# Optimization experiments

Hardware: AMD Instinct MI355X
Metric: run time of the kernel (lower is better)

Reference implementation:

```python
import jax, jax.numpy as jnp
import numpy as np

B, S, HID = 2, 2048, 2048
H, HKV, HD = 16, 8, 128
INPUT_CHUNK, RET_CHUNK = 256, 64
NUM_CHUNKS = S // INPUT_CHUNK - 1          # 7 retrieval chunks
INPUT_START = NUM_CHUNKS * RET_CHUNK       # 448
KV_LEN = S + INPUT_START                   # 2496
SCALE = HD ** -0.5


def _document_id():
    d = np.zeros(KV_LEN, np.int32)
    d[INPUT_START:] = -1
    for i in range(NUM_CHUNKS):            # retrieval chunks get ids 1..NUM_CHUNKS
        d[RET_CHUNK * i: RET_CHUNK * (i + 1)] = i + 1
    for i in range(1, NUM_CHUNKS + 1):     # input chunk i (i>=1) gets id i
        d[INPUT_START + INPUT_CHUNK * i: INPUT_START + INPUT_CHUNK * (i + 1)] = i
    return d


def _causal_retrieval_mask():
    d = _document_id()
    q = np.arange(S)[:, None]
    kv = np.arange(KV_LEN)[None, :]
    causal = (q + INPUT_START >= kv) & (kv > INPUT_START)
    docm = (d[q + INPUT_START] == d[kv]) & (kv < INPUT_START)
    return jnp.asarray(causal | docm)      # [S, KV_LEN] bool


_MASK = _causal_retrieval_mask()


def rotate_half(x):
    x1, x2 = jnp.split(x, 2, axis=-1)
    return jnp.concatenate([-x2, x1], axis=-1)


def setup_inputs() -> dict:
    key = jax.random.key(0)
    ks = jax.random.split(key, 8)
    hidden_states = jax.random.normal(ks[0], (B, S, HID), jnp.float32)
    # standard llama RoPE tables
    pos = jnp.arange(S, dtype=jnp.float32)
    inv = 1.0 / (10000.0 ** (jnp.arange(0, HD, 2, dtype=jnp.float32) / HD))
    f = pos[:, None] * inv[None, :]
    emb = jnp.concatenate([f, f], axis=-1)
    cos = jnp.broadcast_to(jnp.cos(emb), (B, S, HD)).astype(jnp.float32)
    sin = jnp.broadcast_to(jnp.sin(emb), (B, S, HD)).astype(jnp.float32)
    retrieval_key_states = jax.random.normal(ks[1], (B * NUM_CHUNKS, HKV, RET_CHUNK, HD), jnp.float32)
    retrieval_value_states = jax.random.normal(ks[2], (B * NUM_CHUNKS, HKV, RET_CHUNK, HD), jnp.float32)
    s = 0.02
    Wq = jax.random.normal(ks[3], (HID, H * HD), jnp.float32) * s
    Wk = jax.random.normal(ks[4], (HID, HKV * HD), jnp.float32) * s
    Wv = jax.random.normal(ks[5], (HID, HKV * HD), jnp.float32) * s
    Wo = jax.random.normal(ks[6], (H * HD, HID), jnp.float32) * s
    return {"hidden_states": hidden_states, "cos": cos, "sin": sin,
            "retrieval_key_states": retrieval_key_states,
            "retrieval_value_states": retrieval_value_states,
            "Wq": Wq, "Wk": Wk, "Wv": Wv, "Wo": Wo}


def reference(hidden_states, cos, sin, retrieval_key_states, retrieval_value_states, Wq, Wk, Wv, Wo):
    b = hidden_states.shape[0]
    # QKV projections (bias=False), -> [b, h, s, d]
    q = (hidden_states @ Wq).reshape(b, S, H, HD).transpose(0, 2, 1, 3)
    k = (hidden_states @ Wk).reshape(b, S, HKV, HD).transpose(0, 2, 1, 3)
    v = (hidden_states @ Wv).reshape(b, S, HKV, HD).transpose(0, 2, 1, 3)
    # RoPE (cos/sin unsqueezed over heads)
    c = cos[:, None]
    sn = sin[:, None]
    q = q * c + rotate_half(q) * sn
    k = k * c + rotate_half(k) * sn
    # retrieval KV: (b*nc, hkv, rc, d) -> (b, hkv, nc*rc, d)
    rk = retrieval_key_states.reshape(b, NUM_CHUNKS, HKV, RET_CHUNK, HD).transpose(0, 2, 1, 3, 4).reshape(b, HKV, NUM_CHUNKS * RET_CHUNK, HD)
    rv = retrieval_value_states.reshape(b, NUM_CHUNKS, HKV, RET_CHUNK, HD).transpose(0, 2, 1, 3, 4).reshape(b, HKV, NUM_CHUNKS * RET_CHUNK, HD)
    k_all = jnp.concatenate([rk, k], axis=2)     # [b, hkv, KV_LEN, d]
    v_all = jnp.concatenate([rv, v], axis=2)
    # GQA: repeat kv heads
    g = H // HKV
    k_all = jnp.repeat(k_all, g, axis=1)
    v_all = jnp.repeat(v_all, g, axis=1)
    scores = jnp.einsum('bhqd,bhkd->bhqk', q, k_all) * SCALE
    neg = jnp.finfo(scores.dtype).min
    scores = jnp.where(_MASK[None, None], scores, neg)
    probs = jax.nn.softmax(scores, axis=-1)
    # fully-masked rows (q_idx=0) -> 0 output, matching flex_attention semantics
    probs = jnp.where(_MASK[None, None], probs, 0.0)
    attn = jnp.einsum('bhqk,bhkd->bhqd', probs, v_all)   # [b, H, S, HD]
    # NOTE: source reshapes (b, H, S, HD) directly to (b, S, H*HD) with NO transpose
    attn = attn.reshape(b, S, H * HD)
    return attn @ Wo
```

## Files before the change

### kernel.cpp

```cpp
#include <hip/hip_runtime.h>

#define B_ 2
#define S_ 2048
#define HID_ 2048
#define H_ 16
#define HKV_ 8
#define HD_ 128
#define NCH_ 7
#define RET_ 64
#define IST_ 448
#define KVL_ 2496
#define SCALE_ 0.08838834764831845f
#define SC2_ (0.08838834764831845f * 1.44269504088896340f)
#define MCAP_ 16.0f

typedef __attribute__((ext_vector_type(8))) short short8;
typedef __attribute__((ext_vector_type(4))) float f32x4;

static __device__ __forceinline__ unsigned short f2bf(float f) {
    unsigned u = __float_as_uint(f);
    unsigned r = (u + 0x7fffu + ((u >> 16) & 1u)) >> 16;
    return (unsigned short)r;
}
static __device__ __forceinline__ float bf2f(unsigned short x) {
    return __uint_as_float(((unsigned)x) << 16);
}

#define GLL16(gp, lp) __builtin_amdgcn_global_load_lds( \
    (__attribute__((address_space(1))) void*)(void*)(gp), \
    (__attribute__((address_space(3))) void*)(void*)(lp), 16, 0, 0)

__global__ __launch_bounds__(256) void cvt_f32_bf16(const float* __restrict__ x,
                                                    unsigned short* __restrict__ y, int n4) {
    int i = blockIdx.x * 256 + threadIdx.x;
    if (i >= n4) return;
    float4 v = ((const float4*)x)[i];
    ushort4 o;
    o.x = f2bf(v.x); o.y = f2bf(v.y); o.z = f2bf(v.z); o.w = f2bf(v.w);
    ((ushort4*)y)[i] = o;
}

__global__ void transpose_all(const float* __restrict__ Wq, const float* __restrict__ Wk,
                              const float* __restrict__ Wv, const float* __restrict__ Wo,
                              unsigned short* __restrict__ wqkvT, unsigned short* __restrict__ woT) {
    __shared__ float t[32][33];
    const int z = blockIdx.z;
    const float* W;
    unsigned short* WT;
    int N;
    if (z == 0)      { W = Wq; WT = wqkvT;                        N = 2048; }
    else if (z == 1) { W = Wk; WT = wqkvT + (size_t)2048 * 2048;  N = 1024; }
    else if (z == 2) { W = Wv; WT = wqkvT + (size_t)3072 * 2048;  N = 1024; }
    else             { W = Wo; WT = woT;                          N = 2048; }
    const int k0 = blockIdx.x << 5, n0 = blockIdx.y << 5;
    if (n0 >= N) return;
    const int tx = threadIdx.x, ty = threadIdx.y;
#pragma unroll
    for (int i = 0; i < 4; i++)
        t[ty + i * 8][tx] = W[(size_t)(k0 + ty + i * 8) * N + n0 + tx];
    __syncthreads();
#pragma unroll
    for (int i = 0; i < 4; i++)
        WT[(size_t)(n0 + ty + i * 8) * 2048 + k0 + tx] = f2bf(t[tx][ty + i * 8]);
}

template <int BN, typename OT>
__global__ __launch_bounds__(512, 2) void gemm256(const unsigned short* __restrict__ A,
                                                  const unsigned short* __restrict__ BT,
                                                  OT* __restrict__ C,
                                                  int M, int N, int K) {
    constexpr int NJ = BN / 64;
    __shared__ short As[2][16384];
    __shared__ short Bs[2][BN * 64];
    const int tid = threadIdx.x;
    const int wid = tid >> 6, lane = tid & 63;
    const int lq = lane & 15, lk = lane >> 4;
    const int wm = wid >> 2, wn = wid & 3;
    const int bm = blockIdx.x, bn = blockIdx.y;

    const int rowin = tid >> 3;
    const int koff = (((tid & 7) ^ (rowin & 7)) << 3);
    const size_t abase = (size_t)(bm * 256 + rowin) * K;
    const size_t bbase = (size_t)(bn * BN + rowin) * K;
    const int ldst = wid * 512;

    f32x4 acc[8][NJ] = {};

    auto stage = [&](int buf, int k0) {
#pragma unroll
        for (int r = 0; r < 4; r++)
            GLL16(A + abase + (size_t)(r * 64) * K + k0 + koff, &As[buf][r * 4096 + ldst]);
#pragma unroll
        for (int r = 0; r < NJ; r++)
            GLL16(BT + bbase + (size_t)(r * 64) * K + k0 + koff, &Bs[buf][r * 4096 + ldst]);
    };

    const int nk = K >> 6;
    stage(0, 0);
    __syncthreads();
    for (int t = 0; t < nk; t++) {
        const int cur = t & 1;
        if (t + 1 < nk) stage(cur ^ 1, (t + 1) << 6);
        short8 bf[2][NJ];
#pragma unroll
        for (int j = 0; j < NJ; j++)
#pragma unroll
            for (int kk = 0; kk < 2; kk++) {
                const int row = wn * (BN / 4) + j * 16 + lq;
                bf[kk][j] = *(const short8*)&Bs[cur][row * 64 +
                                                     (((kk * 4 + lk) ^ (lq & 7)) << 3)];
            }
#pragma unroll
        for (int p = 0; p < 4; p++) {
            short8 af0[2], af1[2];
#pragma unroll
            for (int kk = 0; kk < 2; kk++) {
                const int r0 = wm * 128 + (2 * p) * 16 + lq;
                const int r1 = wm * 128 + (2 * p + 1) * 16 + lq;
                af0[kk] = *(const short8*)&As[cur][r0 * 64 +
                                                   (((kk * 4 + lk) ^ (lq & 7)) << 3)];
                af1[kk] = *(const short8*)&As[cur][r1 * 64 +
                                                   (((kk * 4 + lk) ^ (lq & 7)) << 3)];
            }
            __builtin_amdgcn_s_setprio(1);
#pragma unroll
            for (int j = 0; j < NJ; j++)
#pragma unroll
                for (int kk = 0; kk < 2; kk++) {
                    acc[2 * p][j] =
                        __builtin_amdgcn_mfma_f32_16x16x32_bf16(bf[kk][j], af0[kk], acc[2 * p][j], 0, 0, 0);
                    acc[2 * p + 1][j] =
                        __builtin_amdgcn_mfma_f32_16x16x32_bf16(bf[kk][j], af1[kk], acc[2 * p + 1][j], 0, 0, 0);
                }
            __builtin_amdgcn_s_setprio(0);
        }
        __syncthreads();
    }
#pragma unroll
    for (int i = 0; i < 8; i++) {
        const size_t row = (size_t)(bm * 256 + wm * 128 + i * 16 + lq);
#pragma unroll
        for (int j = 0; j < NJ; j++) {
            const size_t col = (size_t)(bn * BN + wn * (BN / 4) + j * 16 + lk * 4);
            if constexpr (sizeof(OT) == 2) {
                ushort4 u;
                u.x = f2bf(acc[i][j][0]);
                u.y = f2bf(acc[i][j][1]);
                u.z = f2bf(acc[i][j][2]);
                u.w = f2bf(acc[i][j][3]);
                *(ushort4*)&C[row * N + col] = u;
            } else {
                *(f32x4*)&C[row * N + col] = acc[i][j];
            }
        }
    }
}

__global__ __launch_bounds__(256) void prep_k_kernel(const unsigned short* __restrict__ qkvraw,
                                                     const float* __restrict__ cosb,
                                                     const float* __restrict__ sinb,
                                                     const float* __restrict__ rk,
                                                     unsigned short* __restrict__ kall) {
    const int bid = blockIdx.x;
    if (bid < 8192) {
        size_t idx = (size_t)bid * 256 + threadIdx.x;
        int d = idx & 63;
        int hk = (idx >> 6) & 7;
        size_t bs = idx >> 9;
        size_t base = bs * 4096 + 2048 + hk * 128 + d;
        int b = (int)(bs >> 11), s = (int)(bs & 2047);
        float x1 = bf2f(qkvraw[base]), x2 = bf2f(qkvraw[base + 64]);
        float c1 = cosb[(size_t)s * 128 + d], sn1 = sinb[(size_t)s * 128 + d];
        float c2 = cosb[(size_t)s * 128 + d + 64], sn2 = sinb[(size_t)s * 128 + d + 64];
        size_t o = ((size_t)(b * HKV_ + hk) * KVL_ + IST_ + s) * HD_ + d;
        kall[o] = f2bf(x1 * c1 - x2 * sn1);
        kall[o + 64] = f2bf(x2 * c2 + x1 * sn2);
    } else {
        size_t idx = (size_t)(bid - 8192) * 256 + threadIdx.x;
        int d = idx & 127;
        int r = (idx >> 7) & 63;
        int hk = (idx >> 13) & 7;
        int bc = (int)(idx >> 16);
        int b = bc / NCH_, ch = bc % NCH_;
        kall[((size_t)(b * HKV_ + hk) * KVL_ + ch * RET_ + r) * HD_ + d] = f2bf(rk[idx]);
    }
}

__global__ void prep_v_kernel(const unsigned short* __restrict__ qkvraw,
                              const float* __restrict__ rv,
                              unsigned short* __restrict__ vt) {
    const int bid = blockIdx.x;
    const int tx = threadIdx.x, ty = threadIdx.y;
    if (bid < 4096) {
        __shared__ unsigned short t[32][33];
        const int d0 = (bid & 3) << 5, s0 = ((bid >> 2) & 63) << 5;
        const int bh = bid >> 8;
        const int b = bh >> 3, hk = bh & 7;
#pragma unroll
        for (int i = 0; i < 4; i++)
            t[ty + i * 8][tx] =
                qkvraw[(size_t)(b * S_ + s0 + ty + i * 8) * 4096 + 3072 + hk * 128 + d0 + tx];
        __syncthreads();
#pragma unroll
        for (int i = 0; i < 4; i++)
            vt[((size_t)(b * HKV_ + hk) * HD_ + d0 + ty + i * 8) * KVL_ + IST_ + s0 + tx] =
                t[tx][ty + i * 8];
    } else {
        __shared__ float tf[32][33];
        const int bid2 = bid - 4096;
        const int d0 = (bid2 & 3) << 5;
        const int r0 = ((bid2 >> 2) & 1) << 5;
        const int z = bid2 >> 3;
        const int bc = z >> 3, hk = z & 7;
        const int b = bc / NCH_, ch = bc % NCH_;
#pragma unroll
        for (int i = 0; i < 4; i++)
            tf[ty + i * 8][tx] =
                rv[((size_t)(bc * HKV_ + hk) * RET_ + r0 + ty + i * 8) * HD_ + d0 + tx];
        __syncthreads();
#pragma unroll
        for (int i = 0; i < 4; i++)
            vt[((size_t)(b * HKV_ + hk) * HD_ + d0 + ty + i * 8) * KVL_ + ch * RET_ + r0 + tx] =
                f2bf(tf[tx][ty + i * 8]);
    }
}

__global__ __launch_bounds__(1024) void attn_kernel(const unsigned short* __restrict__ qkvraw,
                                                    const unsigned short* __restrict__ kall,
                                                    const unsigned short* __restrict__ vt,
                                                    const float* __restrict__ cosb,
                                                    const float* __restrict__ sinb,
                                                    unsigned short* __restrict__ attnb) {
    __shared__ short Ks[2][8192];
    __shared__ short Vs[2][8192];
    __shared__ short Ps[16][1024];
    const int tid = threadIdx.x;
    const int wid = tid >> 6, lane = tid & 63;
    const int lq = lane & 15, lk = lane >> 4;
    const int pairi = blockIdx.x;
    const int h = blockIdx.y, b = blockIdx.z, hk = h >> 1;
    const unsigned short* kbase = kall + (size_t)(b * HKV_ + hk) * KVL_ * HD_;
    const unsigned short* vbase = vt + (size_t)(b * HKV_ + hk) * HD_ * KVL_;

    const int so = tid * 16;
    const int krow = so >> 8;
    const int koffe = (((tid & 15) ^ (krow & 7)) << 3);
    const int vrow = so >> 7;
    const unsigned short* vrp = vbase + (size_t)vrow * KVL_ + (((tid & 7) ^ (vrow & 7)) << 3);
    short* psw = &Ps[wid][0];

    const int qlo = pairi * 128, qhi = (15 - pairi) * 128;
    const int wgrp = wid >> 3;
    const int qb0 = wgrp ? qhi : qlo;
    const int qbw = qb0 + (wid & 7) * 16;
    const int mydoc = qb0 >> 8;
    const int doc_lo = qlo >> 8;
    const int doc_hi = qhi >> 8;
    const int nr = (doc_lo >= 1 ? 2 : 1);
    const int nt = nr + (qhi + 128) / 64;

    const unsigned short* qrp = qkvraw + ((size_t)(b * S_) + qbw + lq) * 4096 + h * 128;
    short8 qr[4];
#pragma unroll
    for (int d = 0; d < 4; d++) qr[d] = *(const short8*)(qrp + d * 32 + lk * 8);
    const float* cosp = cosb + (size_t)(qbw + lq) * 128 + lk * 8;
    const float* sinp = sinb + (size_t)(qbw + lq) * 128 + lk * 8;
    short8 qf[4];
#pragma unroll
    for (int d = 0; d < 4; d++) {
        float4 c0 = *(const float4*)(cosp + d * 32);
        float4 c1 = *(const float4*)(cosp + d * 32 + 4);
        float4 s0 = *(const float4*)(sinp + d * 32);
        float4 s1 = *(const float4*)(sinp + d * 32 + 4);
        const float cc[8] = {c0.x, c0.y, c0.z, c0.w, c1.x, c1.y, c1.z, c1.w};
        const float ss[8] = {s0.x, s0.y, s0.z, s0.w, s1.x, s1.y, s1.z, s1.w};
        const int od = d ^ 2;
        const float sg = (d < 2) ? -1.f : 1.f;
#pragma unroll
        for (int e = 0; e < 8; e++) {
            float x = bf2f((unsigned short)qr[d][e]);
            float y = bf2f((unsigned short)qr[od][e]);
            qf[d][e] = (short)f2bf(fmaf(sg * y, ss[e], x * cc[e]));
        }
    }

    f32x4 o[8] = {};
    float lsump = 0.f;

    auto kvof = [&](int t) -> int {
        if (t < nr) return (nr == 2 && t == 0) ? RET_ * (doc_lo - 1) : RET_ * (doc_hi - 1);
        return IST_ + (t - nr) * 64;
    };
    auto stage = [&](int buf, int kv0) {
        GLL16(kbase + (size_t)(kv0 + krow) * HD_ + koffe, &Ks[buf][wid * 512]);
        GLL16(vrp + kv0, &Vs[buf][wid * 512]);
    };

    stage(0, kvof(0));
    asm volatile("s_waitcnt vmcnt(0)" ::: "memory");
    __syncthreads();
    int cur = 0;
    for (int t = 0; t < nt; t++) {
        if (t + 1 < nt) stage(cur ^ 1, kvof(t + 1));
        const int kv0 = kvof(t);
        const bool isret = (kv0 < IST_);
        const bool active = isret ? (mydoc >= 1 && kv0 == RET_ * (mydoc - 1))
                                  : (kv0 <= qbw + 15 + IST_);
        if (active) {
            const bool needMask = !isret && !((kv0 != IST_) && (kv0 + 63 <= qbw + IST_));
            const char* kb = (const char*)&Ks[cur][0];
            const char* vb = (const char*)&Vs[cur][0];
            f32x4 sa[4] = {};
            __builtin_amdgcn_s_setprio(1);
#pragma unroll
            for (int d = 0; d < 4; d++) {
#pragma unroll
                for (int j = 0; j < 4; j++) {
                    short8 kf = *(const short8*)(kb + ((j * 16 + lq) * 256 +
                                                       (((d * 4 + lk) ^ (lq & 7)) << 4)));
                    sa[j] = __builtin_amdgcn_mfma_f32_16x16x32_bf16(kf, qf[d], sa[j], 0, 0, 0);
                }
            }
            __builtin_amdgcn_s_setprio(0);

            if (needMask) {
                const int qg = qbw + lq;
#pragma unroll
                for (int j = 0; j < 4; j++)
#pragma unroll
                    for (int r = 0; r < 4; r++) {
                        int kg = kv0 + j * 16 + lk * 4 + r;
                        if (!(kg > IST_ && kg <= qg + IST_)) sa[j][r] = -3e38f;
                    }
            }
#pragma unroll
            for (int j = 0; j < 4; j++) {
                float p0 = __builtin_amdgcn_exp2f(fmaf(sa[j][0], SC2_, -MCAP_));
                float p1 = __builtin_amdgcn_exp2f(fmaf(sa[j][1], SC2_, -MCAP_));
                float p2 = __builtin_amdgcn_exp2f(fmaf(sa[j][2], SC2_, -MCAP_));
                float p3 = __builtin_amdgcn_exp2f(fmaf(sa[j][3], SC2_, -MCAP_));
                lsump += (p0 + p1) + (p2 + p3);
                uint2 w;
                w.x = ((unsigned)f2bf(p1) << 16) | f2bf(p0);
                w.y = ((unsigned)f2bf(p3) << 16) | f2bf(p2);
                *(uint2*)((char*)psw + (lq * 128 + ((j * 32 + lk * 8) ^ ((lq & 7) << 4)))) = w;
            }
            __builtin_amdgcn_s_setprio(1);
#pragma unroll
            for (int ks = 0; ks < 2; ks++) {
                short8 pa = *(const short8*)((const char*)psw +
                                             (lq * 128 + (((ks * 4 + lk) ^ (lq & 7)) << 4)));
#pragma unroll
                for (int db = 0; db < 8; db++) {
                    short8 vf = *(const short8*)(vb + ((db * 16 + lq) * 128 +
                                                       (((ks * 4 + lk) ^ (lq & 7)) << 4)));
                    o[db] = __builtin_amdgcn_mfma_f32_16x16x32_bf16(pa, vf, o[db], 0, 0, 0);
                }
            }
            __builtin_amdgcn_s_setprio(0);
        }
        if (t + 1 < nt) asm volatile("s_waitcnt vmcnt(0)" ::: "memory");
        __syncthreads();
        cur ^= 1;
    }

    float ls = lsump;
    ls += __shfl_xor(ls, 16);
    ls += __shfl_xor(ls, 32);
    float inv[4];
#pragma unroll
    for (int r = 0; r < 4; r++) {
        float v = __shfl(ls, lk * 4 + r);
        inv[r] = v > 0.f ? 1.f / v : 0.f;
    }
#pragma unroll
    for (int db = 0; db < 8; db++)
#pragma unroll
        for (int r = 0; r < 4; r++) {
            int qg = qbw + lk * 4 + r;
            size_t row = (size_t)b * 2048 + h * 128 + (qg >> 4);
            size_t col = (size_t)(qg & 15) * 128 + db * 16 + lq;
            attnb[row * 2048 + col] = f2bf(o[db][r] * inv[r]);
        }
}

extern "C" void kernel_launch(void* const* d_in, const int* in_sizes, int n_in,
                              void* d_out, int out_size, void* d_ws, size_t ws_size,
                              hipStream_t stream) {
    const float* hidden = (const float*)d_in[0];
    const float* cosb = (const float*)d_in[1];
    const float* sinb = (const float*)d_in[2];
    const float* rk = (const float*)d_in[3];
    const float* rv = (const float*)d_in[4];
    const float* Wq = (const float*)d_in[5];
    const float* Wk = (const float*)d_in[6];
    const float* Wv = (const float*)d_in[7];
    const float* Wo = (const float*)d_in[8];
    float* out = (float*)d_out;

    char* ws = (char*)d_ws;
    unsigned short* hb     = (unsigned short*)(ws + 0);
    unsigned short* wqkvT  = (unsigned short*)(ws + 16777216);
    unsigned short* woT    = (unsigned short*)(ws + 33554432);
    unsigned short* qkvraw = (unsigned short*)(ws + 41943040);
    unsigned short* kallb  = (unsigned short*)(ws + 92274688);
    unsigned short* vtb    = (unsigned short*)(ws + 102498304);
    unsigned short* attnb  = (unsigned short*)(ws + 112721920);

    cvt_f32_bf16<<<8192, 256, 0, stream>>>(hidden, hb, 2097152);
    transpose_all<<<dim3(64, 64, 4), dim3(32, 8), 0, stream>>>(Wq, Wk, Wv, Wo, wqkvT, woT);

    gemm256<256, unsigned short><<<dim3(16, 16), 512, 0, stream>>>(hb, wqkvT, qkvraw, 4096, 4096, 2048);

    prep_k_kernel<<<11776, 256, 0, stream>>>(qkvraw, cosb, sinb, rk, kallb);
    prep_v_kernel<<<4992, dim3(32, 8), 0, stream>>>(qkvraw, rv, vtb);

    attn_kernel<<<dim3(8, 16, 2), 1024, 0, stream>>>(qkvraw, kallb, vtb, cosb, sinb, attnb);

    gemm256<128, float><<<dim3(16, 16), 512, 0, stream>>>(attnb, woT, out, 4096, 2048, 2048);
}
```

Before: 224.1 us.

## Double KV tile to 128 and merge both retrieval chunks into one stage

Doubles the K/V shared-memory tile from 64 to 128 keys per iteration, which halves the number of loop iterations and their barriers. Both retrieval chunks (low and high query group) are loaded together in a single first stage, and each wave group processes only its own half. Softmax and PV are factored into a helper that is applied to each 64-key half. LDS use per block roughly doubles, which may lower occupancy, and causal-masked work is coarser at the diagonal.

```diff
diff --git a/kernel.cpp b/kernel.cpp
--- a/kernel.cpp
+++ b/kernel.cpp
@@ -231,8 +231,8 @@
                                                     const float* __restrict__ cosb,
                                                     const float* __restrict__ sinb,
                                                     unsigned short* __restrict__ attnb) {
-    __shared__ short Ks[2][8192];
-    __shared__ short Vs[2][8192];
+    __shared__ short Ks[2][16384];
+    __shared__ short Vs[2][16384];
     __shared__ short Ps[16][1024];
     const int tid = threadIdx.x;
     const int wid = tid >> 6, lane = tid & 63;
@@ -242,22 +242,24 @@
     const unsigned short* kbase = kall + (size_t)(b * HKV_ + hk) * KVL_ * HD_;
     const unsigned short* vbase = vt + (size_t)(b * HKV_ + hk) * HD_ * KVL_;
 
-    const int so = tid * 16;
-    const int krow = so >> 8;
-    const int koffe = (((tid & 15) ^ (krow & 7)) << 3);
-    const int vrow = so >> 7;
-    const unsigned short* vrp = vbase + (size_t)vrow * KVL_ + (((tid & 7) ^ (vrow & 7)) << 3);
+    int row_[2], xc_[2];
+#pragma unroll
+    for (int p = 0; p < 2; p++) {
+        int o = p * 16384 + tid * 16;
+        row_[p] = o >> 8;
+        xc_[p] = (tid & 15) ^ (row_[p] & 7);
+    }
     short* psw = &Ps[wid][0];
 
     const int qlo = pairi * 128, qhi = (15 - pairi) * 128;
     const int wgrp = wid >> 3;
     const int qb0 = wgrp ? qhi : qlo;
     const int qbw = qb0 + (wid & 7) * 16;
-    const int mydoc = qb0 >> 8;
     const int doc_lo = qlo >> 8;
     const int doc_hi = qhi >> 8;
-    const int nr = (doc_lo >= 1 ? 2 : 1);
-    const int nt = nr + (qhi + 128) / 64;
+    const int kvA = RET_ * ((doc_lo >= 1 ? doc_lo : 1) - 1);
+    const int kvB = RET_ * (doc_hi - 1);
+    const int nt = 17 - pairi;
 
     const unsigned short* qrp = qkvraw + ((size_t)(b * S_) + qbw + lq) * 4096 + h * 128;
     short8 qr[4];
@@ -287,77 +289,107 @@
     f32x4 o[8] = {};
     float lsump = 0.f;
 
-    auto kvof = [&](int t) -> int {
-        if (t < nr) return (nr == 2 && t == 0) ? RET_ * (doc_lo - 1) : RET_ * (doc_hi - 1);
-        return IST_ + (t - nr) * 64;
+    auto stage = [&](int buf, int kv0) {
+#pragma unroll
+        for (int p = 0; p < 2; p++) {
+            GLL16(kbase + (size_t)(kv0 + row_[p]) * HD_ + xc_[p] * 8,
+                  &Ks[buf][p * 8192 + wid * 512]);
+            GLL16(vbase + (size_t)row_[p] * KVL_ + kv0 + xc_[p] * 8,
+                  &Vs[buf][p * 8192 + wid * 512]);
+        }
     };
-    auto stage = [&](int buf, int kv0) {
-        GLL16(kbase + (size_t)(kv0 + krow) * HD_ + koffe, &Ks[buf][wid * 512]);
-        GLL16(vrp + kv0, &Vs[buf][wid * 512]);
+    auto stage_ret = [&](int buf) {
+#pragma unroll
+        for (int p = 0; p < 2; p++) {
+            int kr = row_[p];
+            int ks = (kr < 64) ? kvA + kr : kvB + (kr - 64);
+            GLL16(kbase + (size_t)ks * HD_ + xc_[p] * 8, &Ks[buf][p * 8192 + wid * 512]);
+            int vc = (xc_[p] < 8) ? kvA + xc_[p] * 8 : kvB + (xc_[p] - 8) * 8;
+            GLL16(vbase + (size_t)row_[p] * KVL_ + vc, &Vs[buf][p * 8192 + wid * 512]);
+        }
     };
-
-    stage(0, kvof(0));
+    auto smpv = [&](f32x4* sa4, int hb8, const char* vb) {
+#pragma unroll
+        for (int j2 = 0; j2 < 4; j2++) {
+            float p0 = __builtin_amdgcn_exp2f(fmaf(sa4[j2][0], SC2_, -MCAP_));
+            float p1 = __builtin_amdgcn_exp2f(fmaf(sa4[j2][1], SC2_, -MCAP_));
+            float p2 = __builtin_amdgcn_exp2f(fmaf(sa4[j2][2], SC2_, -MCAP_));
+            float p3 = __builtin_amdgcn_exp2f(fmaf(sa4[j2][3], SC2_, -MCAP_));
+            lsump += (p0 + p1) + (p2 + p3);
+            uint2 w;
+            w.x = ((unsigned)f2bf(p1) << 16) | f2bf(p0);
+            w.y = ((unsigned)f2bf(p3) << 16) | f2bf(p2);
+            *(uint2*)((char*)psw + (lq * 128 + ((j2 * 32 + lk * 8) ^ ((lq & 7) << 4)))) = w;
+        }
+        __builtin_amdgcn_s_setprio(1);
+#pragma unroll
+        for (int ks = 0; ks < 2; ks++) {
+            short8 pa = *(const short8*)((const char*)psw +
+                                         (lq * 128 + (((ks * 4 + lk) ^ (lq & 7)) << 4)));
+#pragma unroll
+            for (int db = 0; db < 8; db++) {
+                short8 vf = *(const short8*)(vb + ((db * 16 + lq) * 256 +
+                                                   (((hb8 + ks * 4 + lk) ^ (lq & 7)) << 4)));
+                o[db] = __builtin_amdgcn_mfma_f32_16x16x32_bf16(pa, vf, o[db], 0, 0, 0);
+            }
+        }
+        __builtin_amdgcn_s_setprio(0);
+    };
+
+    stage_ret(0);
     asm volatile("s_waitcnt vmcnt(0)" ::: "memory");
     __syncthreads();
     int cur = 0;
     for (int t = 0; t < nt; t++) {
-        if (t + 1 < nt) stage(cur ^ 1, kvof(t + 1));
-        const int kv0 = kvof(t);
-        const bool isret = (kv0 < IST_);
-        const bool active = isret ? (mydoc >= 1 && kv0 == RET_ * (mydoc - 1))
-                                  : (kv0 <= qbw + 15 + IST_);
-        if (active) {
-            const bool needMask = !isret && !((kv0 != IST_) && (kv0 + 63 <= qbw + IST_));
-            const char* kb = (const char*)&Ks[cur][0];
-            const char* vb = (const char*)&Vs[cur][0];
-            f32x4 sa[4] = {};
-            __builtin_amdgcn_s_setprio(1);
-#pragma unroll
-            for (int d = 0; d < 4; d++) {
-#pragma unroll
-                for (int j = 0; j < 4; j++) {
-                    short8 kf = *(const short8*)(kb + ((j * 16 + lq) * 256 +
-                                                       (((d * 4 + lk) ^ (lq & 7)) << 4)));
-                    sa[j] = __builtin_amdgcn_mfma_f32_16x16x32_bf16(kf, qf[d], sa[j], 0, 0, 0);
+        if (t + 1 < nt) stage(cur ^ 1, IST_ + t * 128);
+        const char* kb = (const char*)&Ks[cur][0];
+        const char* vb = (const char*)&Vs[cur][0];
+        if (t == 0) {
+            const bool retact = (wgrp == 1) || (doc_lo >= 1);
+            if (retact) {
+                const int hh = wgrp;
+                f32x4 sa[4] = {};
+                __builtin_amdgcn_s_setprio(1);
+#pragma unroll
+                for (int d = 0; d < 4; d++)
+#pragma unroll
+                    for (int j2 = 0; j2 < 4; j2++) {
+                        short8 kf = *(const short8*)(kb + (((hh * 4 + j2) * 16 + lq) * 256 +
+                                                           (((d * 4 + lk) ^ (lq & 7)) << 4)));
+                        sa[j2] = __builtin_amdgcn_mfma_f32_16x16x32_bf16(kf, qf[d], sa[j2], 0, 0, 0);
+                    }
+                __builtin_amdgcn_s_setprio(0);
+                smpv(sa, hh * 8, vb);
+            }
+        } else {
+            const int kv0 = IST_ + (t - 1) * 128;
+            const bool active = kv0 <= qbw + 15 + IST_;
+            if (active) {
+                f32x4 sa[8] = {};
+                __builtin_amdgcn_s_setprio(1);
+#pragma unroll
+                for (int d = 0; d < 4; d++)
+#pragma unroll
+                    for (int j = 0; j < 8; j++) {
+                        short8 kf = *(const short8*)(kb + ((j * 16 + lq) * 256 +
+                                                           (((d * 4 + lk) ^ (lq & 7)) << 4)));
+                        sa[j] = __builtin_amdgcn_mfma_f32_16x16x32_bf16(kf, qf[d], sa[j], 0, 0, 0);
+                    }
+                __builtin_amdgcn_s_setprio(0);
+                const bool needMask = (kv0 == IST_) || (kv0 + 127 > qbw + IST_);
+                if (needMask) {
+                    const int qg = qbw + lq;
+#pragma unroll
+                    for (int j = 0; j < 8; j++)
+#pragma unroll
+                        for (int r = 0; r < 4; r++) {
+                            int kg = kv0 + j * 16 + lk * 4 + r;
+                            if (!(kg > IST_ && kg <= qg + IST_)) sa[j][r] = -3e38f;
+                        }
                 }
-            }
-            __builtin_amdgcn_s_setprio(0);
-
-            if (needMask) {
-                const int qg = qbw + lq;
-#pragma unroll
-                for (int j = 0; j < 4; j++)
-#pragma unroll
-                    for (int r = 0; r < 4; r++) {
-                        int kg = kv0 + j * 16 + lk * 4 + r;
-                        if (!(kg > IST_ && kg <= qg + IST_)) sa[j][r] = -3e38f;
-                    }
-            }
-#pragma unroll
-            for (int j = 0; j < 4; j++) {
-                float p0 = __builtin_amdgcn_exp2f(fmaf(sa[j][0], SC2_, -MCAP_));
-                float p1 = __builtin_amdgcn_exp2f(fmaf(sa[j][1], SC2_, -MCAP_));
-                float p2 = __builtin_amdgcn_exp2f(fmaf(sa[j][2], SC2_, -MCAP_));
-                float p3 = __builtin_amdgcn_exp2f(fmaf(sa[j][3], SC2_, -MCAP_));
-                lsump += (p0 + p1) + (p2 + p3);
-                uint2 w;
-                w.x = ((unsigned)f2bf(p1) << 16) | f2bf(p0);
-                w.y = ((unsigned)f2bf(p3) << 16) | f2bf(p2);
-                *(uint2*)((char*)psw + (lq * 128 + ((j * 32 + lk * 8) ^ ((lq & 7) << 4)))) = w;
-            }
-            __builtin_amdgcn_s_setprio(1);
-#pragma unroll
-            for (int ks = 0; ks < 2; ks++) {
-                short8 pa = *(const short8*)((const char*)psw +
-                                             (lq * 128 + (((ks * 4 + lk) ^ (lq & 7)) << 4)));
-#pragma unroll
-                for (int db = 0; db < 8; db++) {
-                    short8 vf = *(const short8*)(vb + ((db * 16 + lq) * 128 +
-                                                       (((ks * 4 + lk) ^ (lq & 7)) << 4)));
-                    o[db] = __builtin_amdgcn_mfma_f32_16x16x32_bf16(pa, vf, o[db], 0, 0, 0);
-                }
-            }
-            __builtin_amdgcn_s_setprio(0);
+                smpv(&sa[0], 0, vb);
+                smpv(&sa[4], 8, vb);
+            }
         }
         if (t + 1 < nt) asm volatile("s_waitcnt vmcnt(0)" ::: "memory");
         __syncthreads();
```

After: 221.8 us. No clear change (-1.0%).
